# Performance work log

Hardware: AMD Instinct MI355X
Metric: run time of the kernel (lower is better)

Reference implementation:

```python
import jax, jax.numpy as jnp
import numpy as np

NEG_SLOPE = 0.2


def gat_conv(x, edge_index, W, att_src, att_dst, bias, concat):
    # PyG GATConv with add_self_loops=True, negative_slope=0.2
    N = x.shape[0]
    H, C = att_src.shape
    h = (x @ W).reshape(N, H, C)                      # [N, H, C]
    loops = jnp.arange(N, dtype=edge_index.dtype)
    src = jnp.concatenate([edge_index[0], loops])     # [E+N]
    dst = jnp.concatenate([edge_index[1], loops])
    a_src = jnp.einsum('nhc,hc->nh', h, att_src)      # [N, H]
    a_dst = jnp.einsum('nhc,hc->nh', h, att_dst)
    e = jax.nn.leaky_relu(a_src[src] + a_dst[dst], NEG_SLOPE)  # [E+N, H]
    # segment softmax over destination neighborhoods
    e_max = jax.ops.segment_max(e, dst, num_segments=N)        # [N, H]
    e_exp = jnp.exp(e - e_max[dst])
    denom = jax.ops.segment_sum(e_exp, dst, num_segments=N)    # [N, H]
    alpha = e_exp / denom[dst]                                  # [E+N, H]
    msg = h[src] * alpha[:, :, None]                            # [E+N, H, C]
    out = jax.ops.segment_sum(msg, dst, num_segments=N)        # [N, H, C]
    if concat:
        out = out.reshape(N, H * C)
    else:
        out = out.mean(axis=1)
    return out + bias


def setup_inputs() -> dict:
    key = jax.random.key(0)
    ks = jax.random.split(key, 12)
    N, E = 100000, 1600000
    IN, HID, HEADS = 8, 32, 4
    x = jax.random.normal(ks[0], (N, IN), dtype=jnp.float32)
    edge_index = jax.random.randint(ks[1], (2, E), 0, N, dtype=jnp.int32)
    s = 0.1
    W1 = jax.random.normal(ks[2], (IN, HEADS * HID), dtype=jnp.float32) * s
    att_src1 = jax.random.normal(ks[3], (HEADS, HID), dtype=jnp.float32) * s
    att_dst1 = jax.random.normal(ks[4], (HEADS, HID), dtype=jnp.float32) * s
    bias1 = jnp.zeros((HEADS * HID,), dtype=jnp.float32)
    W2 = jax.random.normal(ks[5], (HEADS * HID, HEADS * HID), dtype=jnp.float32) * s
    att_src2 = jax.random.normal(ks[6], (HEADS, HID), dtype=jnp.float32) * s
    att_dst2 = jax.random.normal(ks[7], (HEADS, HID), dtype=jnp.float32) * s
    bias2 = jnp.zeros((HID,), dtype=jnp.float32)
    W_lin = jax.random.normal(ks[8], (HID, 1), dtype=jnp.float32) * s
    b_lin = jnp.zeros((1,), dtype=jnp.float32)
    return {"x": x, "edge_index": edge_index,
            "W1": W1, "att_src1": att_src1, "att_dst1": att_dst1, "bias1": bias1,
            "W2": W2, "att_src2": att_src2, "att_dst2": att_dst2, "bias2": bias2,
            "W_lin": W_lin, "b_lin": b_lin}


def reference(x, edge_index, W1, att_src1, att_dst1, bias1,
              W2, att_src2, att_dst2, bias2, W_lin, b_lin):
    h = gat_conv(x, edge_index, W1, att_src1, att_dst1, bias1, concat=True)
    h = jax.nn.relu(h)
    # dropout p=0.2 is a no-op in eval mode
    h = gat_conv(h, edge_index, W2, att_src2, att_dst2, bias2, concat=False)
    h = jax.nn.relu(h)
    out = h @ W_lin + b_lin
    return out.reshape(-1)
```

## Files before the change

### kernel.cpp

```cpp
#include <hip/hip_runtime.h>

#define NEG_SLOPE 0.2f
#define K1 1024
#define S1B 512

typedef __attribute__((ext_vector_type(8))) short bf16x8;
typedef __attribute__((ext_vector_type(4))) float f32x4;

__device__ __forceinline__ unsigned short f2b(float f) {
    unsigned int u = __float_as_uint(f);
    u += 0x7FFFu + ((u >> 16) & 1u);
    return (unsigned short)(u >> 16);
}
__device__ __forceinline__ float blo(unsigned int u) { return __uint_as_float(u << 16); }
__device__ __forceinline__ float bhi(unsigned int u) { return __uint_as_float(u & 0xFFFF0000u); }

__global__ __launch_bounds__(256) void k_hist(
    const int* __restrict__ ei, int E, int EN,
    int* __restrict__ counts_t,
    const float* __restrict__ x, const float* __restrict__ W1,
    const float* __restrict__ as1, const float* __restrict__ ad1,
    float* __restrict__ asrc, float* __restrict__ adst,
    const float* __restrict__ W2, unsigned short* __restrict__ W2p,
    int N, int AB)
{
    int b = blockIdx.x;
    int t = threadIdx.x;
    if (b < S1B) {
        __shared__ int h[K1];
        for (int k = t; k < K1; k += 256) h[k] = 0;
        __syncthreads();
        int chunk = (EN + S1B - 1) / S1B;
        int lo = b * chunk, hi = min(lo + chunk, EN);
        for (int e = lo + t; e < hi; e += 256) {
            int dst = (e < E) ? ei[E + e] : (e - E);
            atomicAdd(&h[dst >> 7], 1);
        }
        __syncthreads();
        for (int k = t; k < K1; k += 256)
            counts_t[(size_t)k * S1B + b] = h[k];
        return;
    }
    if (b < S1B + AB) {
        __shared__ float s_wa[32], s_wd[32];
        if (t < 32) {
            int k = t >> 2, hh = t & 3;
            float sa = 0.f, sd = 0.f;
            for (int cc = 0; cc < 32; cc++) {
                float w = W1[k * 128 + hh * 32 + cc];
                sa = fmaf(w, as1[hh * 32 + cc], sa);
                sd = fmaf(w, ad1[hh * 32 + cc], sd);
            }
            s_wa[t] = sa;
            s_wd[t] = sd;
        }
        __syncthreads();
        int g = (b - S1B) * 256 + t;
        int n = g >> 2;
        if (n >= N) return;
        int hh = g & 3;
        const float* xr = x + (size_t)n * 8;
        float sa = 0.f, sd = 0.f;
        #pragma unroll
        for (int k = 0; k < 8; k++) {
            float xv = xr[k];
            sa = fmaf(xv, s_wa[k * 4 + hh], sa);
            sd = fmaf(xv, s_wd[k * 4 + hh], sd);
        }
        asrc[n * 4 + hh] = sa;
        adst[n * 4 + hh] = sd;
        return;
    }
    int w = t >> 6, lane = t & 63;
    int quad = lane >> 4, lanelo = lane & 15;
    int tile_n = b - S1B - AB;
    size_t base = (((size_t)tile_n * 4 + w) * 64 + lane) * 8;
    #pragma unroll
    for (int j = 0; j < 8; j++) {
        int k = w * 32 + quad * 8 + j;
        int n = tile_n * 16 + lanelo;
        W2p[base + j] = f2b(W2[k * 128 + n]);
    }
}

__global__ __launch_bounds__(S1B) void k_cscan(
    int* __restrict__ counts_t, int* __restrict__ T)
{
    __shared__ int s[S1B];
    int k = blockIdx.x, t = threadIdx.x;
    int v = counts_t[(size_t)k * S1B + t];
    s[t] = v;
    __syncthreads();
    for (int off = 1; off < S1B; off <<= 1) {
        int u = (t >= off) ? s[t - off] : 0;
        __syncthreads();
        s[t] += u;
        __syncthreads();
    }
    counts_t[(size_t)k * S1B + t] = s[t] - v;
    if (t == S1B - 1) T[k] = s[t];
}

__global__ __launch_bounds__(K1) void k_tscan(
    const int* __restrict__ T, int* __restrict__ Tofs)
{
    __shared__ int s[K1];
    int t = threadIdx.x;
    int v = T[t];
    s[t] = v;
    __syncthreads();
    for (int off = 1; off < K1; off <<= 1) {
        int u = (t >= off) ? s[t - off] : 0;
        __syncthreads();
        s[t] += u;
        __syncthreads();
    }
    Tofs[t] = s[t] - v;
    if (t == K1 - 1) Tofs[K1] = s[t];
}

__global__ __launch_bounds__(256) void k_place2(
    const int* __restrict__ ei, int E, int EN,
    const int* __restrict__ counts_t, const int* __restrict__ Tofs,
    int2* __restrict__ tmp)
{
    __shared__ int cur[K1];
    int b = blockIdx.x, t = threadIdx.x;
    for (int k = t; k < K1; k += 256)
        cur[k] = Tofs[k] + counts_t[(size_t)k * S1B + b];
    __syncthreads();
    int chunk = (EN + S1B - 1) / S1B;
    int lo = b * chunk, hi = min(lo + chunk, EN);
    for (int e = lo + t; e < hi; e += 256) {
        int src, dst;
        if (e < E) { src = ei[e]; dst = ei[E + e]; }
        else       { src = dst = e - E; }
        int pos = atomicAdd(&cur[dst >> 7], 1);
        tmp[pos] = make_int2(src, dst);
    }
}

__global__ __launch_bounds__(256) void k_fine(
    const int2* __restrict__ tmp, const int* __restrict__ Tofs,
    int* __restrict__ esrc, int* __restrict__ rowptr, int N, int EN)
{
    __shared__ int hist[128], scn[128];
    int k = blockIdx.x, t = threadIdx.x;
    int lo = Tofs[k], hi = Tofs[k + 1];
    if (t < 128) hist[t] = 0;
    __syncthreads();
    for (int i = lo + t; i < hi; i += 256)
        atomicAdd(&hist[tmp[i].y & 127], 1);
    __syncthreads();
    int v = (t < 128) ? hist[t] : 0;
    if (t < 128) scn[t] = v;
    __syncthreads();
    for (int off = 1; off < 128; off <<= 1) {
        int u = (t >= off && t < 128) ? scn[t - off] : 0;
        __syncthreads();
        if (t < 128) scn[t] += u;
        __syncthreads();
    }
    if (t < 128) {
        int ofs = scn[t] - v;
        int dst = (k << 7) + t;
        if (dst < N) rowptr[dst] = lo + ofs;
        hist[t] = ofs;
    }
    if (k == 0 && t == 0) rowptr[N] = EN;
    __syncthreads();
    for (int i = lo + t; i < hi; i += 256) {
        int2 e = tmp[i];
        int r = atomicAdd(&hist[e.y & 127], 1);
        esrc[lo + r] = e.x;
    }
}

__global__ __launch_bounds__(256) void k_l1f2(
    const int* __restrict__ rowptr, const int* __restrict__ esrc,
    const float* __restrict__ x,
    const float* __restrict__ asrc1, const float* __restrict__ adst1,
    const float* __restrict__ W1, const float* __restrict__ bias1,
    const unsigned short* __restrict__ W2p,
    const float* __restrict__ att_src, const float* __restrict__ att_dst,
    unsigned short* __restrict__ h, float* __restrict__ asrc2,
    float* __restrict__ adst2, int N)
{
    __shared__ float s_y[32][36];
    __shared__ float s_d[32][4];
    __shared__ uint4 s_tile[512];
    char* s_a = reinterpret_cast<char*>(s_tile);
    int t = threadIdx.x;
    int mbase = blockIdx.x * 32;

    {
        int nl = t >> 3;
        int node = mbase + nl;
        if (node >= N) node = N - 1;
        int l8 = t & 7;
        int hh = l8 >> 1;
        int dh = (l8 & 1) << 2;
        float ad = adst1[node * 4 + hh];
        float a0 = 0.f, a1 = 0.f, a2 = 0.f, a3 = 0.f, d = 0.f;
        int j = rowptr[node], end = rowptr[node + 1];
        for (; j + 8 <= end; j += 8) {
            int s[8];
            #pragma unroll
            for (int i = 0; i < 8; i++) s[i] = esrc[j + i];
            float A[8];
            #pragma unroll
            for (int i = 0; i < 8; i++) A[i] = asrc1[s[i] * 4 + hh];
            float4 xv[8];
            #pragma unroll
            for (int i = 0; i < 8; i++)
                xv[i] = *reinterpret_cast<const float4*>(x + (size_t)s[i] * 8 + dh);
            #pragma unroll
            for (int i = 0; i < 8; i++) {
                float a = A[i] + ad;
                a = a > 0.f ? a : NEG_SLOPE * a;
                float w = __expf(a);
                a0 = fmaf(w, xv[i].x, a0); a1 = fmaf(w, xv[i].y, a1);
                a2 = fmaf(w, xv[i].z, a2); a3 = fmaf(w, xv[i].w, a3); d += w;
            }
        }
        if (j + 4 <= end) {
            int s[4];
            #pragma unroll
            for (int i = 0; i < 4; i++) s[i] = esrc[j + i];
            float A[4];
            #pragma unroll
            for (int i = 0; i < 4; i++) A[i] = asrc1[s[i] * 4 + hh];
            float4 xv[4];
            #pragma unroll
            for (int i = 0; i < 4; i++)
                xv[i] = *reinterpret_cast<const float4*>(x + (size_t)s[i] * 8 + dh);
            #pragma unroll
            for (int i = 0; i < 4; i++) {
                float a = A[i] + ad;
                a = a > 0.f ? a : NEG_SLOPE * a;
                float w = __expf(a);
                a0 = fmaf(w, xv[i].x, a0); a1 = fmaf(w, xv[i].y, a1);
                a2 = fmaf(w, xv[i].z, a2); a3 = fmaf(w, xv[i].w, a3); d += w;
            }
            j += 4;
        }
        for (; j < end; j++) {
            int src = esrc[j];
            float a = asrc1[src * 4 + hh] + ad;
            a = a > 0.f ? a : NEG_SLOPE * a;
            float w = __expf(a);
            float4 xv = *reinterpret_cast<const float4*>(x + (size_t)src * 8 + dh);
            a0 = fmaf(w, xv.x, a0); a1 = fmaf(w, xv.y, a1);
            a2 = fmaf(w, xv.z, a2); a3 = fmaf(w, xv.w, a3); d += w;
        }
        float4 o = {a0, a1, a2, a3};
        *reinterpret_cast<float4*>(&s_y[nl][l8 * 4]) = o;
        if (dh == 0) s_d[nl][hh] = d;
    }
    __syncthreads();

    {
        int nl = t >> 3;
        int seg = t & 7;
        int head = seg >> 1;
        float inv = 1.f / s_d[nl][head];
        float y8[8];
        #pragma unroll
        for (int k = 0; k < 8; k++) y8[k] = s_y[nl][head * 8 + k];
        int c0 = seg * 16;
        float acc16[16];
        #pragma unroll
        for (int c = 0; c < 16; c++) acc16[c] = 0.f;
        #pragma unroll
        for (int k = 0; k < 8; k++) {
            float yk = y8[k];
            const float4* wr = reinterpret_cast<const float4*>(W1 + k * 128 + c0);
            #pragma unroll
            for (int q = 0; q < 4; q++) {
                float4 wv = wr[q];
                acc16[q * 4 + 0] = fmaf(yk, wv.x, acc16[q * 4 + 0]);
                acc16[q * 4 + 1] = fmaf(yk, wv.y, acc16[q * 4 + 1]);
                acc16[q * 4 + 2] = fmaf(yk, wv.z, acc16[q * 4 + 2]);
                acc16[q * 4 + 3] = fmaf(yk, wv.w, acc16[q * 4 + 3]);
            }
        }
        unsigned int dw[8];
        #pragma unroll
        for (int c = 0; c < 8; c++) {
            float v0 = acc16[2 * c]     * inv + bias1[c0 + 2 * c];
            float v1 = acc16[2 * c + 1] * inv + bias1[c0 + 2 * c + 1];
            v0 = v0 > 0.f ? v0 : 0.f;
            v1 = v1 > 0.f ? v1 : 0.f;
            dw[c] = ((unsigned int)f2b(v1) << 16) | f2b(v0);
        }
        int byte0 = nl * 256 + seg * 32;
        int swz = (nl & 7) << 4;
        *reinterpret_cast<uint4*>(&s_a[byte0 ^ swz]) =
            make_uint4(dw[0], dw[1], dw[2], dw[3]);
        *reinterpret_cast<uint4*>(&s_a[(byte0 + 16) ^ swz]) =
            make_uint4(dw[4], dw[5], dw[6], dw[7]);
    }
    __syncthreads();

    int w = t >> 6;
    int lane = t & 63;
    int quad = lane >> 4, lanelo = lane & 15;
    int wcb = w * 32;

    f32x4 acc[2][2];
    #pragma unroll
    for (int rt = 0; rt < 2; rt++)
        #pragma unroll
        for (int ct = 0; ct < 2; ct++)
            acc[rt][ct] = (f32x4){0.f, 0.f, 0.f, 0.f};

    #pragma unroll
    for (int kc = 0; kc < 4; kc++) {
        bf16x8 a[2], b[2];
        #pragma unroll
        for (int rt = 0; rt < 2; rt++) {
            int nl = rt * 16 + lanelo;
            int byte = nl * 256 + kc * 64 + quad * 16;
            a[rt] = *reinterpret_cast<const bf16x8*>(&s_a[byte ^ ((nl & 7) << 4)]);
        }
        #pragma unroll
        for (int ct = 0; ct < 2; ct++) {
            int tile_n = w * 2 + ct;
            b[ct] = *reinterpret_cast<const bf16x8*>(
                W2p + (((size_t)tile_n * 4 + kc) * 64 + lane) * 8);
        }
        #pragma unroll
        for (int rt = 0; rt < 2; rt++)
            #pragma unroll
            for (int ct = 0; ct < 2; ct++)
                acc[rt][ct] = __builtin_amdgcn_mfma_f32_16x16x32_bf16(
                    a[rt], b[ct], acc[rt][ct], 0, 0, 0);
    }

    float as_[2], ad_[2];
    #pragma unroll
    for (int ct = 0; ct < 2; ct++) {
        int col = wcb + ct * 16 + lanelo;
        as_[ct] = att_src[col];
        ad_[ct] = att_dst[col];
    }
    #pragma unroll
    for (int rt = 0; rt < 2; rt++) {
        #pragma unroll
        for (int reg = 0; reg < 4; reg++) {
            int node = mbase + rt * 16 + quad * 4 + reg;
            bool ok = node < N;
            float v0 = acc[rt][0][reg], v1 = acc[rt][1][reg];
            if (ok) {
                h[(size_t)node * 128 + wcb + lanelo]      = f2b(v0);
                h[(size_t)node * 128 + wcb + 16 + lanelo] = f2b(v1);
            }
            float ps = v0 * as_[0] + v1 * as_[1];
            float pd = v0 * ad_[0] + v1 * ad_[1];
            #pragma unroll
            for (int off = 8; off >= 1; off >>= 1) {
                ps += __shfl_xor(ps, off, 64);
                pd += __shfl_xor(pd, off, 64);
            }
            if (ok && lanelo == 0) {
                asrc2[node * 4 + w] = ps;
                adst2[node * 4 + w] = pd;
            }
        }
    }
}

__device__ __forceinline__ void agg_edge(float w, uint4 u, float acc[8])
{
    acc[0] = fmaf(w, blo(u.x), acc[0]); acc[1] = fmaf(w, bhi(u.x), acc[1]);
    acc[2] = fmaf(w, blo(u.y), acc[2]); acc[3] = fmaf(w, bhi(u.y), acc[3]);
    acc[4] = fmaf(w, blo(u.z), acc[4]); acc[5] = fmaf(w, bhi(u.z), acc[5]);
    acc[6] = fmaf(w, blo(u.w), acc[6]); acc[7] = fmaf(w, bhi(u.w), acc[7]);
}

__device__ __forceinline__ void agg_core16(
    int n, int l4,
    const int* __restrict__ rowptr, const int* __restrict__ esrc,
    const uint4* __restrict__ h ,
    const float* __restrict__ asrc, const float* __restrict__ adst,
    float acc[8], float& d)
{
    int head = l4 >> 2;
    float ad = adst[n * 4 + head];
    #pragma unroll
    for (int k = 0; k < 8; k++) acc[k] = 0.f;
    d = 0.f;
    int j = rowptr[n], end = rowptr[n + 1];

    for (; j + 4 <= end; j += 4) {
        int s0 = esrc[j], s1 = esrc[j + 1], s2 = esrc[j + 2], s3 = esrc[j + 3];
        float A0 = asrc[s0 * 4 + head];
        float A1 = asrc[s1 * 4 + head];
        float A2 = asrc[s2 * 4 + head];
        float A3 = asrc[s3 * 4 + head];
        uint4 u0 = h[(size_t)s0 * 16 + l4];
        uint4 u1 = h[(size_t)s1 * 16 + l4];
        uint4 u2 = h[(size_t)s2 * 16 + l4];
        uint4 u3 = h[(size_t)s3 * 16 + l4];
        A0 += ad; A0 = A0 > 0.f ? A0 : NEG_SLOPE * A0; float w0 = __expf(A0);
        A1 += ad; A1 = A1 > 0.f ? A1 : NEG_SLOPE * A1; float w1 = __expf(A1);
        A2 += ad; A2 = A2 > 0.f ? A2 : NEG_SLOPE * A2; float w2 = __expf(A2);
        A3 += ad; A3 = A3 > 0.f ? A3 : NEG_SLOPE * A3; float w3 = __expf(A3);
        agg_edge(w0, u0, acc); d += w0;
        agg_edge(w1, u1, acc); d += w1;
        agg_edge(w2, u2, acc); d += w2;
        agg_edge(w3, u3, acc); d += w3;
    }
    for (; j < end; j++) {
        int src = esrc[j];
        float a = asrc[src * 4 + head] + ad;
        a = a > 0.f ? a : NEG_SLOPE * a;
        float w = __expf(a);
        uint4 u = h[(size_t)src * 16 + l4];
        agg_edge(w, u, acc); d += w;
    }
}

__global__ __launch_bounds__(256) void k_agg2(
    const int* __restrict__ rowptr, const int* __restrict__ esrc,
    const uint4* __restrict__ h, const float* __restrict__ asrc,
    const float* __restrict__ adst, const float* __restrict__ bias2,
    const float* __restrict__ Wlin, const float* __restrict__ blin,
    float* __restrict__ out, int N)
{
    int gid = blockIdx.x * 256 + threadIdx.x;
    int node = gid >> 4;
    if (node >= N) return;
    int l4 = threadIdx.x & 15;
    float acc[8], d;
    agg_core16(node, l4, rowptr, esrc, h, asrc, adst, acc, d);
    float inv = 1.f / d;
    float v[8];
    #pragma unroll
    for (int k = 0; k < 8; k++) v[k] = acc[k] * inv;
    #pragma unroll
    for (int k = 0; k < 8; k++) {
        v[k] += __shfl_xor(v[k], 4, 64);
        v[k] += __shfl_xor(v[k], 8, 64);
    }
    int cc = (l4 & 3) * 8;
    const float4 b0 = *reinterpret_cast<const float4*>(bias2 + cc);
    const float4 b1 = *reinterpret_cast<const float4*>(bias2 + cc + 4);
    const float4 w0 = *reinterpret_cast<const float4*>(Wlin + cc);
    const float4 w1 = *reinterpret_cast<const float4*>(Wlin + cc + 4);
    float bb[8] = {b0.x, b0.y, b0.z, b0.w, b1.x, b1.y, b1.z, b1.w};
    float ww[8] = {w0.x, w0.y, w0.z, w0.w, w1.x, w1.y, w1.z, w1.w};
    float t = 0.f;
    #pragma unroll
    for (int k = 0; k < 8; k++) {
        float m = 0.25f * v[k] + bb[k];
        float y = m > 0.f ? m : 0.f;
        t = fmaf(y, ww[k], t);
    }
    t += __shfl_xor(t, 1, 64);
    t += __shfl_xor(t, 2, 64);
    if (l4 == 0) out[node] = t + blin[0];
}

extern "C" void kernel_launch(void* const* d_in, const int* in_sizes, int n_in,
                              void* d_out, int out_size, void* d_ws, size_t ws_size,
                              hipStream_t stream)
{
    const float* x   = (const float*)d_in[0];
    const int*   ei  = (const int*)  d_in[1];
    const float* W1  = (const float*)d_in[2];
    const float* as1 = (const float*)d_in[3];
    const float* ad1 = (const float*)d_in[4];
    const float* b1  = (const float*)d_in[5];
    const float* W2  = (const float*)d_in[6];
    const float* as2 = (const float*)d_in[7];
    const float* ad2 = (const float*)d_in[8];
    const float* b2  = (const float*)d_in[9];
    const float* Wl  = (const float*)d_in[10];
    const float* bl  = (const float*)d_in[11];
    float* out = (float*)d_out;

    int N  = in_sizes[0] / 8;
    int E  = in_sizes[1] / 2;
    int EN = E + N;

    float* ws    = (float*)d_ws;
    unsigned short* A = (unsigned short*)ws;
    float* asrc1 = ws + (size_t)N * 64;
    float* adst1 = asrc1 + (size_t)N * 4;
    float* asrc2 = adst1 + (size_t)N * 4;
    float* adst2 = asrc2 + (size_t)N * 4;
    int* rowptr  = (int*)(adst2 + (size_t)N * 4);
    int* esrc    = rowptr + (N + 1);
    int* counts_t = esrc + EN;
    int* T       = counts_t + (size_t)K1 * S1B;
    int* Tofs    = T + K1;
    unsigned short* W2p = (unsigned short*)(Tofs + K1 + 1);
    uintptr_t tp = (uintptr_t)(W2p + 16384);
    tp = (tp + 7) & ~(uintptr_t)7;
    int2* tmp    = (int2*)tp;

    int ab = (N + 63) / 64;
    int nb = (N + 15) / 16;

    k_hist<<<S1B + ab + 8, 256, 0, stream>>>(ei, E, EN, counts_t,
                                             x, W1, as1, ad1, asrc1, adst1,
                                             W2, W2p, N, ab);
    k_cscan<<<K1, S1B, 0, stream>>>(counts_t, T);
    k_tscan<<<1, K1, 0, stream>>>(T, Tofs);
    k_place2<<<S1B, 256, 0, stream>>>(ei, E, EN, counts_t, Tofs, tmp);
    k_fine<<<K1, 256, 0, stream>>>(tmp, Tofs, esrc, rowptr, N, EN);

    k_l1f2<<<(N + 31) / 32, 256, 0, stream>>>(rowptr, esrc, x, asrc1, adst1,
                                              W1, b1, W2p, as2, ad2,
                                              A, asrc2, adst2, N);
    k_agg2<<<nb, 256, 0, stream>>>(rowptr, esrc, (const uint4*)A,
                                   asrc2, adst2, b2, Wl, bl, out, N);
}
```

Measured before the change: 269.1 us.

## Fuse bucket-total scan into consumers, pack edge pairs, merge fine sort with layer-1

Drops the single-block bucket-total scan kernel; each place and fine-sort block now redundantly scans the 1024 bucket totals in shared memory. Edge pairs in the temporary buffer are packed into one 32-bit word (src<<7 | dst&127), halving that traffic. The fine CSR sort is merged with the layer-1 aggregation and W2 projection, so each 128-node bucket block builds its rows and then processes four 32-node subtiles using row starts held in shared memory. This removes two launches and a round trip through the row pointers, but the fused kernel has only 1024 blocks doing serial subtile work, which lowers parallelism and occupancy compared with the earlier ~3125-block layer-1 launch.

After: 343.0 us. 27.4% more time.

```diff
diff --git a/kernel.cpp b/kernel.cpp
--- a/kernel.cpp
+++ b/kernel.cpp
@@ -101,33 +101,40 @@
     if (t == S1B - 1) T[k] = s[t];
 }
 
-__global__ __launch_bounds__(K1) void k_tscan(
-    const int* __restrict__ T, int* __restrict__ Tofs)
-{
-    __shared__ int s[K1];
-    int t = threadIdx.x;
-    int v = T[t];
-    s[t] = v;
-    __syncthreads();
-    for (int off = 1; off < K1; off <<= 1) {
-        int u = (t >= off) ? s[t - off] : 0;
-        __syncthreads();
-        s[t] += u;
-        __syncthreads();
-    }
-    Tofs[t] = s[t] - v;
-    if (t == K1 - 1) Tofs[K1] = s[t];
+__device__ __forceinline__ void tofs_scan(const int* __restrict__ T,
+                                          int* sT, int* ps, int t)
+{
+    int base = t * 4;
+    int s0 = T[base], s1 = T[base + 1], s2 = T[base + 2], s3 = T[base + 3];
+    int tot = s0 + s1 + s2 + s3;
+    ps[t] = tot;
+    __syncthreads();
+    for (int off = 1; off < 256; off <<= 1) {
+        int u = (t >= off) ? ps[t - off] : 0;
+        __syncthreads();
+        ps[t] += u;
+        __syncthreads();
+    }
+    int excl = ps[t] - tot;
+    sT[base]     = excl;
+    sT[base + 1] = excl + s0;
+    sT[base + 2] = excl + s0 + s1;
+    sT[base + 3] = excl + s0 + s1 + s2;
+    __syncthreads();
 }
 
 __global__ __launch_bounds__(256) void k_place2(
     const int* __restrict__ ei, int E, int EN,
-    const int* __restrict__ counts_t, const int* __restrict__ Tofs,
-    int2* __restrict__ tmp)
-{
+    const int* __restrict__ counts_t, const int* __restrict__ T,
+    unsigned int* __restrict__ tmp)
+{
+    __shared__ int sT[K1];
+    __shared__ int ps[256];
     __shared__ int cur[K1];
     int b = blockIdx.x, t = threadIdx.x;
+    tofs_scan(T, sT, ps, t);
     for (int k = t; k < K1; k += 256)
-        cur[k] = Tofs[k] + counts_t[(size_t)k * S1B + b];
+        cur[k] = sT[k] + counts_t[(size_t)k * S1B + b];
     __syncthreads();
     int chunk = (EN + S1B - 1) / S1B;
     int lo = b * chunk, hi = min(lo + chunk, EN);
@@ -136,237 +143,250 @@
         if (e < E) { src = ei[e]; dst = ei[E + e]; }
         else       { src = dst = e - E; }
         int pos = atomicAdd(&cur[dst >> 7], 1);
-        tmp[pos] = make_int2(src, dst);
-    }
-}
-
-__global__ __launch_bounds__(256) void k_fine(
-    const int2* __restrict__ tmp, const int* __restrict__ Tofs,
-    int* __restrict__ esrc, int* __restrict__ rowptr, int N, int EN)
-{
-    __shared__ int hist[128], scn[128];
-    int k = blockIdx.x, t = threadIdx.x;
-    int lo = Tofs[k], hi = Tofs[k + 1];
-    if (t < 128) hist[t] = 0;
-    __syncthreads();
-    for (int i = lo + t; i < hi; i += 256)
-        atomicAdd(&hist[tmp[i].y & 127], 1);
-    __syncthreads();
-    int v = (t < 128) ? hist[t] : 0;
-    if (t < 128) scn[t] = v;
-    __syncthreads();
-    for (int off = 1; off < 128; off <<= 1) {
-        int u = (t >= off && t < 128) ? scn[t - off] : 0;
-        __syncthreads();
-        if (t < 128) scn[t] += u;
-        __syncthreads();
-    }
-    if (t < 128) {
-        int ofs = scn[t] - v;
-        int dst = (k << 7) + t;
-        if (dst < N) rowptr[dst] = lo + ofs;
-        hist[t] = ofs;
-    }
-    if (k == 0 && t == 0) rowptr[N] = EN;
-    __syncthreads();
-    for (int i = lo + t; i < hi; i += 256) {
-        int2 e = tmp[i];
-        int r = atomicAdd(&hist[e.y & 127], 1);
-        esrc[lo + r] = e.x;
-    }
-}
-
-__global__ __launch_bounds__(256) void k_l1f2(
-    const int* __restrict__ rowptr, const int* __restrict__ esrc,
+        tmp[pos] = ((unsigned int)src << 7) | (unsigned int)(dst & 127);
+    }
+}
+
+__global__ __launch_bounds__(256) void k_fl(
+    const unsigned int* __restrict__ tmp, const int* __restrict__ T,
+    int* __restrict__ esrc, int* __restrict__ rowptr,
     const float* __restrict__ x,
     const float* __restrict__ asrc1, const float* __restrict__ adst1,
     const float* __restrict__ W1, const float* __restrict__ bias1,
     const unsigned short* __restrict__ W2p,
     const float* __restrict__ att_src, const float* __restrict__ att_dst,
     unsigned short* __restrict__ h, float* __restrict__ asrc2,
-    float* __restrict__ adst2, int N)
-{
+    float* __restrict__ adst2, int N, int EN)
+{
+    __shared__ int sT[K1];
+    __shared__ int ps[256];
+    __shared__ int hist[128], scn[128];
+    __shared__ int s_start[128], s_cnt[128];
     __shared__ float s_y[32][36];
     __shared__ float s_d[32][4];
     __shared__ uint4 s_tile[512];
     char* s_a = reinterpret_cast<char*>(s_tile);
-    int t = threadIdx.x;
-    int mbase = blockIdx.x * 32;
-
-    {
-        int nl = t >> 3;
-        int node = mbase + nl;
-        if (node >= N) node = N - 1;
-        int l8 = t & 7;
-        int hh = l8 >> 1;
-        int dh = (l8 & 1) << 2;
-        float ad = adst1[node * 4 + hh];
-        float a0 = 0.f, a1 = 0.f, a2 = 0.f, a3 = 0.f, d = 0.f;
-        int j = rowptr[node], end = rowptr[node + 1];
-        for (; j + 8 <= end; j += 8) {
-            int s[8];
-            #pragma unroll
-            for (int i = 0; i < 8; i++) s[i] = esrc[j + i];
-            float A[8];
-            #pragma unroll
-            for (int i = 0; i < 8; i++) A[i] = asrc1[s[i] * 4 + hh];
-            float4 xv[8];
-            #pragma unroll
-            for (int i = 0; i < 8; i++)
-                xv[i] = *reinterpret_cast<const float4*>(x + (size_t)s[i] * 8 + dh);
-            #pragma unroll
-            for (int i = 0; i < 8; i++) {
-                float a = A[i] + ad;
+    int k = blockIdx.x, t = threadIdx.x;
+
+    tofs_scan(T, sT, ps, t);
+    int lo = sT[k];
+    int hi = (k == K1 - 1) ? EN : sT[k + 1];
+    int nbase = k << 7;
+    if (k == K1 - 1 && t == 0) rowptr[N] = EN;
+    if (nbase >= N) return;
+
+    if (t < 128) hist[t] = 0;
+    __syncthreads();
+    for (int i = lo + t; i < hi; i += 256)
+        atomicAdd(&hist[tmp[i] & 127], 1);
+    __syncthreads();
+    int v = (t < 128) ? hist[t] : 0;
+    if (t < 128) scn[t] = v;
+    __syncthreads();
+    for (int off = 1; off < 128; off <<= 1) {
+        int u = (t >= off && t < 128) ? scn[t - off] : 0;
+        __syncthreads();
+        if (t < 128) scn[t] += u;
+        __syncthreads();
+    }
+    if (t < 128) {
+        int ofs = scn[t] - v;
+        int dst = nbase + t;
+        if (dst < N) rowptr[dst] = lo + ofs;
+        s_start[t] = lo + ofs;
+        s_cnt[t] = v;
+        hist[t] = ofs;
+    }
+    __syncthreads();
+    for (int i = lo + t; i < hi; i += 256) {
+        unsigned int e = tmp[i];
+        int r = atomicAdd(&hist[e & 127], 1);
+        esrc[lo + r] = (int)(e >> 7);
+    }
+    __syncthreads();
+
+    for (int sub = 0; sub < 4; sub++) {
+        int mbase = nbase + sub * 32;
+        {
+            int nl = t >> 3;
+            int li = sub * 32 + nl;
+            int node = mbase + nl;
+            if (node >= N) {
+                node = N - 1;
+                li = (N - 1) - nbase;
+            }
+            int l8 = t & 7;
+            int hh = l8 >> 1;
+            int dh = (l8 & 1) << 2;
+            float ad = adst1[node * 4 + hh];
+            float a0 = 0.f, a1 = 0.f, a2 = 0.f, a3 = 0.f, d = 0.f;
+            int j = s_start[li], end = j + s_cnt[li];
+            for (; j + 8 <= end; j += 8) {
+                int s[8];
+                #pragma unroll
+                for (int i = 0; i < 8; i++) s[i] = esrc[j + i];
+                float A[8];
+                #pragma unroll
+                for (int i = 0; i < 8; i++) A[i] = asrc1[s[i] * 4 + hh];
+                float4 xv[8];
+                #pragma unroll
+                for (int i = 0; i < 8; i++)
+                    xv[i] = *reinterpret_cast<const float4*>(x + (size_t)s[i] * 8 + dh);
+                #pragma unroll
+                for (int i = 0; i < 8; i++) {
+                    float a = A[i] + ad;
+                    a = a > 0.f ? a : NEG_SLOPE * a;
+                    float w = __expf(a);
+                    a0 = fmaf(w, xv[i].x, a0); a1 = fmaf(w, xv[i].y, a1);
+                    a2 = fmaf(w, xv[i].z, a2); a3 = fmaf(w, xv[i].w, a3); d += w;
+                }
+            }
+            if (j + 4 <= end) {
+                int s[4];
+                #pragma unroll
+                for (int i = 0; i < 4; i++) s[i] = esrc[j + i];
+                float A[4];
+                #pragma unroll
+                for (int i = 0; i < 4; i++) A[i] = asrc1[s[i] * 4 + hh];
+                float4 xv[4];
+                #pragma unroll
+                for (int i = 0; i < 4; i++)
+                    xv[i] = *reinterpret_cast<const float4*>(x + (size_t)s[i] * 8 + dh);
+                #pragma unroll
+                for (int i = 0; i < 4; i++) {
+                    float a = A[i] + ad;
+                    a = a > 0.f ? a : NEG_SLOPE * a;
+                    float w = __expf(a);
+                    a0 = fmaf(w, xv[i].x, a0); a1 = fmaf(w, xv[i].y, a1);
+                    a2 = fmaf(w, xv[i].z, a2); a3 = fmaf(w, xv[i].w, a3); d += w;
+                }
+                j += 4;
+            }
+            for (; j < end; j++) {
+                int src = esrc[j];
+                float a = asrc1[src * 4 + hh] + ad;
                 a = a > 0.f ? a : NEG_SLOPE * a;
                 float w = __expf(a);
-                a0 = fmaf(w, xv[i].x, a0); a1 = fmaf(w, xv[i].y, a1);
-                a2 = fmaf(w, xv[i].z, a2); a3 = fmaf(w, xv[i].w, a3); d += w;
-            }
-        }
-        if (j + 4 <= end) {
-            int s[4];
-            #pragma unroll
-            for (int i = 0; i < 4; i++) s[i] = esrc[j + i];
-            float A[4];
-            #pragma unroll
-            for (int i = 0; i < 4; i++) A[i] = asrc1[s[i] * 4 + hh];
-            float4 xv[4];
-            #pragma unroll
-            for (int i = 0; i < 4; i++)
-                xv[i] = *reinterpret_cast<const float4*>(x + (size_t)s[i] * 8 + dh);
-            #pragma unroll
-            for (int i = 0; i < 4; i++) {
-                float a = A[i] + ad;
-                a = a > 0.f ? a : NEG_SLOPE * a;
-                float w = __expf(a);
-                a0 = fmaf(w, xv[i].x, a0); a1 = fmaf(w, xv[i].y, a1);
-                a2 = fmaf(w, xv[i].z, a2); a3 = fmaf(w, xv[i].w, a3); d += w;
-            }
-            j += 4;
-        }
-        for (; j < end; j++) {
-            int src = esrc[j];
-            float a = asrc1[src * 4 + hh] + ad;
-            a = a > 0.f ? a : NEG_SLOPE * a;
-            float w = __expf(a);
-            float4 xv = *reinterpret_cast<const float4*>(x + (size_t)src * 8 + dh);
-            a0 = fmaf(w, xv.x, a0); a1 = fmaf(w, xv.y, a1);
-            a2 = fmaf(w, xv.z, a2); a3 = fmaf(w, xv.w, a3); d += w;
-        }
-        float4 o = {a0, a1, a2, a3};
-        *reinterpret_cast<float4*>(&s_y[nl][l8 * 4]) = o;
-        if (dh == 0) s_d[nl][hh] = d;
-    }
-    __syncthreads();
-
-    {
-        int nl = t >> 3;
-        int seg = t & 7;
-        int head = seg >> 1;
-        float inv = 1.f / s_d[nl][head];
-        float y8[8];
+                float4 xv = *reinterpret_cast<const float4*>(x + (size_t)src * 8 + dh);
+                a0 = fmaf(w, xv.x, a0); a1 = fmaf(w, xv.y, a1);
+                a2 = fmaf(w, xv.z, a2); a3 = fmaf(w, xv.w, a3); d += w;
+            }
+            float4 o = {a0, a1, a2, a3};
+            *reinterpret_cast<float4*>(&s_y[nl][l8 * 4]) = o;
+            if (dh == 0) s_d[nl][hh] = d;
+        }
+        __syncthreads();
+
+        {
+            int nl = t >> 3;
+            int seg = t & 7;
+            int head = seg >> 1;
+            float inv = 1.f / s_d[nl][head];
+            float y8[8];
+            #pragma unroll
+            for (int kk = 0; kk < 8; kk++) y8[kk] = s_y[nl][head * 8 + kk];
+            int c0 = seg * 16;
+            float acc16[16];
+            #pragma unroll
+            for (int c = 0; c < 16; c++) acc16[c] = 0.f;
+            #pragma unroll
+            for (int kk = 0; kk < 8; kk++) {
+                float yk = y8[kk];
+                const float4* wr = reinterpret_cast<const float4*>(W1 + kk * 128 + c0);
+                #pragma unroll
+                for (int q = 0; q < 4; q++) {
+                    float4 wv = wr[q];
+                    acc16[q * 4 + 0] = fmaf(yk, wv.x, acc16[q * 4 + 0]);
+                    acc16[q * 4 + 1] = fmaf(yk, wv.y, acc16[q * 4 + 1]);
+                    acc16[q * 4 + 2] = fmaf(yk, wv.z, acc16[q * 4 + 2]);
+                    acc16[q * 4 + 3] = fmaf(yk, wv.w, acc16[q * 4 + 3]);
+                }
+            }
+            unsigned int dw[8];
+            #pragma unroll
+            for (int c = 0; c < 8; c++) {
+                float v0 = acc16[2 * c]     * inv + bias1[c0 + 2 * c];
+                float v1 = acc16[2 * c + 1] * inv + bias1[c0 + 2 * c + 1];
+                v0 = v0 > 0.f ? v0 : 0.f;
+                v1 = v1 > 0.f ? v1 : 0.f;
+                dw[c] = ((unsigned int)f2b(v1) << 16) | f2b(v0);
+            }
+            int byte0 = nl * 256 + seg * 32;
+            int swz = (nl & 7) << 4;
+            *reinterpret_cast<uint4*>(&s_a[byte0 ^ swz]) =
+                make_uint4(dw[0], dw[1], dw[2], dw[3]);
+            *reinterpret_cast<uint4*>(&s_a[(byte0 + 16) ^ swz]) =
+                make_uint4(dw[4], dw[5], dw[6], dw[7]);
+        }
+        __syncthreads();
+
+        int w = t >> 6;
+        int lane = t & 63;
+        int quad = lane >> 4, lanelo = lane & 15;
+        int wcb = w * 32;
+
+        f32x4 acc[2][2];
         #pragma unroll
-        for (int k = 0; k < 8; k++) y8[k] = s_y[nl][head * 8 + k];
-        int c0 = seg * 16;
-        float acc16[16];
+        for (int rt = 0; rt < 2; rt++)
+            #pragma unroll
+            for (int ct = 0; ct < 2; ct++)
+                acc[rt][ct] = (f32x4){0.f, 0.f, 0.f, 0.f};
+
         #pragma unroll
-        for (int c = 0; c < 16; c++) acc16[c] = 0.f;
+        for (int kc = 0; kc < 4; kc++) {
+            bf16x8 a[2], b[2];
+            #pragma unroll
+            for (int rt = 0; rt < 2; rt++) {
+                int nl = rt * 16 + lanelo;
+                int byte = nl * 256 + kc * 64 + quad * 16;
+                a[rt] = *reinterpret_cast<const bf16x8*>(&s_a[byte ^ ((nl & 7) << 4)]);
+            }
+            #pragma unroll
+            for (int ct = 0; ct < 2; ct++) {
+                int tile_n = w * 2 + ct;
+                b[ct] = *reinterpret_cast<const bf16x8*>(
+                    W2p + (((size_t)tile_n * 4 + kc) * 64 + lane) * 8);
+            }
+            #pragma unroll
+            for (int rt = 0; rt < 2; rt++)
+                #pragma unroll
+                for (int ct = 0; ct < 2; ct++)
+                    acc[rt][ct] = __builtin_amdgcn_mfma_f32_16x16x32_bf16(
+                        a[rt], b[ct], acc[rt][ct], 0, 0, 0);
+        }
+
+        float as_[2], ad_[2];
         #pragma unroll
-        for (int k = 0; k < 8; k++) {
-            float yk = y8[k];
-            const float4* wr = reinterpret_cast<const float4*>(W1 + k * 128 + c0);
-            #pragma unroll
-            for (int q = 0; q < 4; q++) {
-                float4 wv = wr[q];
-                acc16[q * 4 + 0] = fmaf(yk, wv.x, acc16[q * 4 + 0]);
-                acc16[q * 4 + 1] = fmaf(yk, wv.y, acc16[q * 4 + 1]);
-                acc16[q * 4 + 2] = fmaf(yk, wv.z, acc16[q * 4 + 2]);
-                acc16[q * 4 + 3] = fmaf(yk, wv.w, acc16[q * 4 + 3]);
-            }
-        }
-        unsigned int dw[8];
-        #pragma unroll
-        for (int c = 0; c < 8; c++) {
-            float v0 = acc16[2 * c]     * inv + bias1[c0 + 2 * c];
-            float v1 = acc16[2 * c + 1] * inv + bias1[c0 + 2 * c + 1];
-            v0 = v0 > 0.f ? v0 : 0.f;
-            v1 = v1 > 0.f ? v1 : 0.f;
-            dw[c] = ((unsigned int)f2b(v1) << 16) | f2b(v0);
-        }
-        int byte0 = nl * 256 + seg * 32;
-        int swz = (nl & 7) << 4;
-        *reinterpret_cast<uint4*>(&s_a[byte0 ^ swz]) =
-            make_uint4(dw[0], dw[1], dw[2], dw[3]);
-        *reinterpret_cast<uint4*>(&s_a[(byte0 + 16) ^ swz]) =
-            make_uint4(dw[4], dw[5], dw[6], dw[7]);
-    }
-    __syncthreads();
-
-    int w = t >> 6;
-    int lane = t & 63;
-    int quad = lane >> 4, lanelo = lane & 15;
-    int wcb = w * 32;
-
-    f32x4 acc[2][2];
-    #pragma unroll
-    for (int rt = 0; rt < 2; rt++)
-        #pragma unroll
-        for (int ct = 0; ct < 2; ct++)
-            acc[rt][ct] = (f32x4){0.f, 0.f, 0.f, 0.f};
-
-    #pragma unroll
-    for (int kc = 0; kc < 4; kc++) {
-        bf16x8 a[2], b[2];
+        for (int ct = 0; ct < 2; ct++) {
+            int col = wcb + ct * 16 + lanelo;
+            as_[ct] = att_src[col];
+            ad_[ct] = att_dst[col];
+        }
         #pragma unroll
         for (int rt = 0; rt < 2; rt++) {
-            int nl = rt * 16 + lanelo;
-            int byte = nl * 256 + kc * 64 + quad * 16;
-            a[rt] = *reinterpret_cast<const bf16x8*>(&s_a[byte ^ ((nl & 7) << 4)]);
-        }
-        #pragma unroll
-        for (int ct = 0; ct < 2; ct++) {
-            int tile_n = w * 2 + ct;
-            b[ct] = *reinterpret_cast<const bf16x8*>(
-                W2p + (((size_t)tile_n * 4 + kc) * 64 + lane) * 8);
-        }
-        #pragma unroll
-        for (int rt = 0; rt < 2; rt++)
-            #pragma unroll
-            for (int ct = 0; ct < 2; ct++)
-                acc[rt][ct] = __builtin_amdgcn_mfma_f32_16x16x32_bf16(
-                    a[rt], b[ct], acc[rt][ct], 0, 0, 0);
-    }
-
-    float as_[2], ad_[2];
-    #pragma unroll
-    for (int ct = 0; ct < 2; ct++) {
-        int col = wcb + ct * 16 + lanelo;
-        as_[ct] = att_src[col];
-        ad_[ct] = att_dst[col];
-    }
-    #pragma unroll
-    for (int rt = 0; rt < 2; rt++) {
-        #pragma unroll
-        for (int reg = 0; reg < 4; reg++) {
-            int node = mbase + rt * 16 + quad * 4 + reg;
-            bool ok = node < N;
-            float v0 = acc[rt][0][reg], v1 = acc[rt][1][reg];
-            if (ok) {
-                h[(size_t)node * 128 + wcb + lanelo]      = f2b(v0);
-                h[(size_t)node * 128 + wcb + 16 + lanelo] = f2b(v1);
-            }
-            float ps = v0 * as_[0] + v1 * as_[1];
-            float pd = v0 * ad_[0] + v1 * ad_[1];
-            #pragma unroll
-            for (int off = 8; off >= 1; off >>= 1) {
-                ps += __shfl_xor(ps, off, 64);
-                pd += __shfl_xor(pd, off, 64);
-            }
-            if (ok && lanelo == 0) {
-                asrc2[node * 4 + w] = ps;
-                adst2[node * 4 + w] = pd;
-            }
-        }
+            #pragma unroll
+            for (int reg = 0; reg < 4; reg++) {
+                int node = mbase + rt * 16 + quad * 4 + reg;
+                bool ok = node < N;
+                float v0 = acc[rt][0][reg], v1 = acc[rt][1][reg];
+                if (ok) {
+                    h[(size_t)node * 128 + wcb + lanelo]      = f2b(v0);
+                    h[(size_t)node * 128 + wcb + 16 + lanelo] = f2b(v1);
+                }
+                float psum = v0 * as_[0] + v1 * as_[1];
+                float pdum = v0 * ad_[0] + v1 * ad_[1];
+                #pragma unroll
+                for (int off = 8; off >= 1; off >>= 1) {
+                    psum += __shfl_xor(psum, off, 64);
+                    pdum += __shfl_xor(pdum, off, 64);
+                }
+                if (ok && lanelo == 0) {
+                    asrc2[node * 4 + w] = psum;
+                    adst2[node * 4 + w] = pdum;
+                }
+            }
+        }
+        __syncthreads();
     }
 }
 
@@ -494,11 +514,8 @@
     int* esrc    = rowptr + (N + 1);
     int* counts_t = esrc + EN;
     int* T       = counts_t + (size_t)K1 * S1B;
-    int* Tofs    = T + K1;
-    unsigned short* W2p = (unsigned short*)(Tofs + K1 + 1);
-    uintptr_t tp = (uintptr_t)(W2p + 16384);
-    tp = (tp + 7) & ~(uintptr_t)7;
-    int2* tmp    = (int2*)tp;
+    unsigned short* W2p = (unsigned short*)(T + K1);
+    unsigned int* tmp = (unsigned int*)(W2p + 16384);
 
     int ab = (N + 63) / 64;
     int nb = (N + 15) / 16;
@@ -507,13 +524,9 @@
                                              x, W1, as1, ad1, asrc1, adst1,
                                              W2, W2p, N, ab);
     k_cscan<<<K1, S1B, 0, stream>>>(counts_t, T);
-    k_tscan<<<1, K1, 0, stream>>>(T, Tofs);
-    k_place2<<<S1B, 256, 0, stream>>>(ei, E, EN, counts_t, Tofs, tmp);
-    k_fine<<<K1, 256, 0, stream>>>(tmp, Tofs, esrc, rowptr, N, EN);
-
-    k_l1f2<<<(N + 31) / 32, 256, 0, stream>>>(rowptr, esrc, x, asrc1, adst1,
-                                              W1, b1, W2p, as2, ad2,
-                                              A, asrc2, adst2, N);
+    k_place2<<<S1B, 256, 0, stream>>>(ei, E, EN, counts_t, T, tmp);
+    k_fl<<<K1, 256, 0, stream>>>(tmp, T, esrc, rowptr, x, asrc1, adst1,
+                                 W1, b1, W2p, as2, ad2, A, asrc2, adst2, N, EN);
     k_agg2<<<nb, 256, 0, stream>>>(rowptr, esrc, (const uint4*)A,
                                    asrc2, adst2, b2, Wl, bl, out, N);
 }
```
